# Kernel tuning notes

Measured on AMD Instinct MI355X. Metric: run time of the kernel, lower is better.

Reference implementation:

```python
import jax, jax.numpy as jnp
import numpy as np

EPS = 1e-12  # F.normalize eps

def _unfold3(x):
    # x: [B,C,H,W] -> [B, C*9, H*W], matching F.unfold(kernel=3, padding=1)
    B, C, H, W = x.shape
    xp = jnp.pad(x, ((0, 0), (0, 0), (1, 1), (1, 1)))
    pats = jnp.stack([xp[:, :, i:i + H, j:j + W]
                      for i in range(3) for j in range(3)], axis=2)  # [B,C,9,H,W]
    return pats.reshape(B, C * 9, H * W)

def _fold3(t, H, W):
    # inverse of _unfold3 with overlap-add, matching F.fold(kernel=3, padding=1)
    B, CK, L = t.shape
    C = CK // 9
    t = t.reshape(B, C, 3, 3, H, W)
    out = jnp.zeros((B, C, H + 2, W + 2), t.dtype)
    for i in range(3):
        for j in range(3):
            out = out.at[:, :, i:i + H, j:j + W].add(t[:, :, i, j])
    return out[:, :, 1:1 + H, 1:1 + W]

def setup_inputs() -> dict:
    key = jax.random.key(0)
    kV, kK, kQ = jax.random.split(key, 3)
    B, C, H, W = 4, 64, 64, 64
    return {
        'V': jax.random.normal(kV, (B, C, H, W), dtype=jnp.float32),
        'K': jax.random.normal(kK, (B, C, H, W), dtype=jnp.float32),
        'Q': jax.random.normal(kQ, (B, C, H, W), dtype=jnp.float32),
    }

def reference(V, K, Q):
    B, C, H, W = Q.shape
    Qu = _unfold3(Q)  # [B, C9, L]
    Ku = _unfold3(K)  # [B, C9, L]
    # F.normalize along the feature (C*9) axis for both K (after permute dim=2) and Q (dim=1)
    Kn = Ku / jnp.maximum(jnp.linalg.norm(Ku, axis=1, keepdims=True), EPS)
    Qn = Qu / jnp.maximum(jnp.linalg.norm(Qu, axis=1, keepdims=True), EPS)
    # R[b,k,q] = <Kn[b,:,k], Qn[b,:,q]>  -> [B, L, L]
    R = jnp.einsum('bfk,bfq->bkq', Kn, Qn)
    S = jnp.max(R, axis=1)        # [B, L]
    arg = jnp.argmax(R, axis=1)   # [B, L] best key patch per query position
    Vu = _unfold3(V)              # [B, C9, L]
    idx = jnp.broadcast_to(arg[:, None, :], Vu.shape)
    T_unfold = jnp.take_along_axis(Vu, idx, axis=2)  # gather along patch dim
    T = _fold3(T_unfold, H, W) / 9.0                 # [B, C, H, W]
    S = S.reshape(B, 1, H, W)
    return (S, T)
```

## Files before the change

### kernel.cpp

```cpp
#include <hip/hip_runtime.h>
#include <math.h>

#define HW 4096

typedef short bf16x8 __attribute__((ext_vector_type(8)));
typedef float floatx4 __attribute__((ext_vector_type(4)));
typedef unsigned short u16x8 __attribute__((ext_vector_type(8)));

__device__ __forceinline__ unsigned short f2bf_rne(float x) {
    unsigned int u = __float_as_uint(x);
    unsigned int r = (u + 0x7FFFu + ((u >> 16) & 1u)) >> 16;
    return (unsigned short)r;
}
__device__ __forceinline__ float bf2f(unsigned short h) {
    return __uint_as_float(((unsigned int)h) << 16);
}

__device__ __forceinline__ void gload_lds16(const void* gptr, void* lptr) {
    auto g = (const __attribute__((address_space(1))) unsigned int*)(unsigned long long)(gptr);
    auto l = (__attribute__((address_space(3))) unsigned int*)(unsigned int)(unsigned long long)(lptr);
    __builtin_amdgcn_global_load_lds(g, l, 16, 0, 0);
}

__global__ __launch_bounds__(256)
void prep_kernel(const float* __restrict__ Q, const float* __restrict__ K,
                 unsigned short* __restrict__ Aq, unsigned short* __restrict__ Bq,
                 float* __restrict__ pix2q, float* __restrict__ pix2k) {
    __shared__ float sT[64][65];
    const int tid = threadIdx.x;
    const int p0 = blockIdx.x * 64;
    const int b = blockIdx.y;
    const int isK = blockIdx.z;
    const float* __restrict__ src = isK ? K : Q;
    unsigned short* __restrict__ dst = isK ? Bq : Aq;
    float* __restrict__ pix2 = isK ? pix2k : pix2q;
    const int pp = tid >> 2, qt = tid & 3;
    const size_t base = ((size_t)b * 4096 + p0 + pp) * 192;

#pragma unroll
    for (int it = 0; it < 16; ++it) {
        int idx = it * 256 + tid;
        int c = idx >> 6, x = idx & 63;
        sT[c][x] = src[((size_t)b * 64 + c) * HW + p0 + x];
    }
    __syncthreads();
    {
        float sq = 0.f;
        u16x8 hv[2], lv[2];
#pragma unroll
        for (int g = 0; g < 2; ++g)
#pragma unroll
            for (int j = 0; j < 8; ++j) {
                int c = qt * 16 + g * 8 + j;
                float x = sT[c][pp];
                sq = fmaf(x, x, sq);
                unsigned short h = f2bf_rne(x);
                hv[g][j] = h;
                lv[g][j] = f2bf_rne(x - bf2f(h));
            }
        sq += __shfl_xor(sq, 1, 64);
        sq += __shfl_xor(sq, 2, 64);
        if (qt == 0) pix2[(b << 12) + p0 + pp] = sq;
#pragma unroll
        for (int g = 0; g < 2; ++g) {
            int co = qt * 16 + g * 8;
            *(u16x8*)(dst + base + co)       = hv[g];
            *(u16x8*)(dst + base + 64 + co)  = isK ? lv[g] : hv[g];
            *(u16x8*)(dst + base + 128 + co) = isK ? hv[g] : lv[g];
        }
    }
}

__global__ void patchnorm_kernel(const float* __restrict__ pix2q, const float* __restrict__ pix2k,
                                 float* __restrict__ rnq, float* __restrict__ rnk) {
    int idx = blockIdx.x * 256 + threadIdx.x;
    int b = idx >> 12, p = idx & 4095;
    int py = p >> 6, px = p & 63;
    float sq = 0.f, sk = 0.f;
    for (int dy = -1; dy <= 1; ++dy)
        for (int dx = -1; dx <= 1; ++dx) {
            int yy = py + dy, xx = px + dx;
            if ((unsigned)yy < 64u && (unsigned)xx < 64u) {
                int o = (b << 12) + (yy << 6) + xx;
                sq += pix2q[o];
                sk += pix2k[o];
            }
        }
    rnq[idx] = 1.f / fmaxf(sqrtf(sq), 1e-12f);
    rnk[idx] = 1.f / fmaxf(sqrtf(sk), 1e-12f);
}

#define WAITV(n_) asm volatile("s_waitcnt vmcnt(" #n_ ")" ::: "memory")
#define PBAR(n_) do { WAITV(n_); __builtin_amdgcn_s_barrier(); \
                      asm volatile("" ::: "memory"); } while (0)

#define ISSUE_A(c_, sg_, slot_) do { \
    const char* g_ = Aqb + (size_t)(q0 - 64 + (c_) * 64) * 384 + (sg_) * 128; \
    gload_lds16(g_ + g0off, smem + (slot_) * 8192 + l0off); \
    gload_lds16(g_ + g1off, smem + (slot_) * 8192 + l1off); \
} while (0)
#define ISSUE_B(c_, sg_, slot_) do { \
    const char* g_ = Bqb + (size_t)(k0 - 64 + (c_) * 64) * 384 + (sg_) * 128; \
    gload_lds16(g_ + g0off, smemB + (slot_) * 8192 + l0off); \
    gload_lds16(g_ + g1off, smemB + (slot_) * 8192 + l1off); \
} while (0)

#define MM16(af_, bfr_) do { \
    __builtin_amdgcn_s_setprio(1); \
    _Pragma("unroll") \
    for (int mt = 0; mt < 4; ++mt) \
        _Pragma("unroll") \
        for (int nt = 0; nt < 4; ++nt) \
            acc[mt][nt] = __builtin_amdgcn_mfma_f32_16x16x32_bf16( \
                (af_)[mt], (bfr_)[nt], acc[mt][nt], 0, 0, 0); \
    __builtin_amdgcn_s_setprio(0); \
} while (0)

#define STEP_S0(D_) do { \
    const char* As_ = smem + (wm + (D_)) * 8192; \
    const char* Bs_ = smemB + (wn + (D_)) * 8192; \
    _Pragma("unroll") \
    for (int kk = 0; kk < 2; ++kk) { \
        const int pk_ = kk ? posK1 : posK0; \
        _Pragma("unroll") \
        for (int mt = 0; mt < 4; ++mt) \
            afc[kk][mt] = *(const bf16x8*)(As_ + mt * 2048 + rowB + pk_); \
        _Pragma("unroll") \
        for (int nt = 0; nt < 4; ++nt) \
            bfc[kk][nt] = *(const bf16x8*)(Bs_ + nt * 2048 + rowB + pk_); \
        MM16(afc[kk], bfc[kk]); \
    } \
} while (0)

#define STEP_S1(D_) do { \
    const int xb_ = wn + (D_); \
    const char* Bs_ = smemB + (xb_ < 2 ? xb_ + 3 : xb_ - 2) * 8192; \
    _Pragma("unroll") \
    for (int kk = 0; kk < 2; ++kk) { \
        const int pk_ = kk ? posK1 : posK0; \
        bf16x8 bfr[4]; \
        _Pragma("unroll") \
        for (int nt = 0; nt < 4; ++nt) \
            bfr[nt] = *(const bf16x8*)(Bs_ + nt * 2048 + rowB + pk_); \
        MM16(afc[kk], bfr); \
    } \
} while (0)

#define STEP_S2(D_) do { \
    const int xa_ = wm + (D_); \
    const char* As_ = smem + ((xa_ & 1) ? (xa_ >> 1) : 4) * 8192; \
    _Pragma("unroll") \
    for (int kk = 0; kk < 2; ++kk) { \
        const int pk_ = kk ? posK1 : posK0; \
        bf16x8 af[4]; \
        _Pragma("unroll") \
        for (int mt = 0; mt < 4; ++mt) \
            af[mt] = *(const bf16x8*)(As_ + mt * 2048 + rowB + pk_); \
        MM16(af, bfc[kk]); \
    } \
} while (0)

__global__ __launch_bounds__(256, 2)
void gemm_fused_kernel(const unsigned short* __restrict__ Aq, const unsigned short* __restrict__ Bq,
                       const float* __restrict__ rnkA,
                       float* __restrict__ part_val, int* __restrict__ part_arg) {
    __shared__ __align__(16) char smem[81920];
    char* const smemB = smem + 40960;
    const int tid = threadIdx.x;
    const int lane = tid & 63, wid = tid >> 6;
    const int m15 = lane & 15, quad = lane >> 4;
    const int wm = wid & 1, wn = wid >> 1;
    const int f = blockIdx.x + (blockIdx.y << 5);
    const int o = ((f & 7) << 7) + (f >> 3);
    const int kt = o & 31, qt = o >> 5;
    const int k0 = kt << 7;
    const int q0 = qt << 7;
    const int b = blockIdx.z;
    const char* Aqb = (const char*)(Aq + (size_t)b * 4096 * 192);
    const char* Bqb = (const char*)(Bq + (size_t)b * 4096 * 192);
    const bool aInt = (q0 >= 64) && (q0 <= 4096 - 192);
    const bool bInt = (k0 >= 64) && (k0 <= 4096 - 192);

    const int rr0 = tid >> 3, ps = tid & 7;
    const int g0off = rr0 * 384 + (ps ^ (rr0 & 7)) * 16;
    const int l0off = tid * 16;
    const int rr1 = (256 + tid) >> 3;
    const int g1off = rr1 * 384 + (ps ^ (rr1 & 7)) * 16;
    const int l1off = (256 + tid) * 16;
    const int rowB = m15 * 128;
    const int posK0 = (quad ^ (m15 & 7)) * 16;
    const int posK1 = ((4 + quad) ^ (m15 & 7)) * 16;

    floatx4 acc[4][4];
#pragma unroll
    for (int i = 0; i < 4; ++i)
#pragma unroll
        for (int j = 0; j < 4; ++j) acc[i][j] = (floatx4)0.f;

    bf16x8 afc[2][4];
    bf16x8 bfc[2][4];

    if (aInt && bInt) {
        ISSUE_A(0, 0, 0); ISSUE_A(1, 0, 1); ISSUE_B(0, 0, 0); ISSUE_B(1, 0, 1);
        ISSUE_A(2, 0, 2); ISSUE_B(2, 0, 2); ISSUE_A(3, 0, 3); ISSUE_B(0, 1, 3);
        ISSUE_B(1, 1, 4); ISSUE_A(0, 2, 4);
        PBAR(12);                                      STEP_S0(0);
        PBAR(2);  ISSUE_A(1, 2, 0); ISSUE_B(2, 1, 0); STEP_S1(0);
        PBAR(2);  ISSUE_B(3, 0, 3);                   STEP_S2(0);
        PBAR(14); ISSUE_A(2, 2, 4);                   STEP_S0(1);
        PBAR(4);  ISSUE_B(3, 1, 1);                   STEP_S1(1);
        PBAR(2);  ISSUE_A(3, 2, 1);                   STEP_S2(1);
        PBAR(6);                                      STEP_S0(2);
        PBAR(2);                                      STEP_S1(2);
        PBAR(0);                                      STEP_S2(2);
        __syncthreads();
    } else {
        for (int seg = 0; seg < 3; ++seg) {
            const char* abL = Aqb + (size_t)(q0 - 64) * 384 + seg * 128;
            const char* bbL = Bqb + (size_t)(k0 - 64) * 384 + seg * 128;
            if (aInt) {
#pragma unroll
                for (int it = 0; it < 8; ++it) {
                    int slot = it * 256 + tid;
                    int row = slot >> 3, pos = slot & 7;
                    int G = pos ^ (row & 7);
                    gload_lds16(abL + (size_t)row * 384 + G * 16, smem + slot * 16);
                }
            } else {
#pragma unroll
                for (int it = 0; it < 8; ++it) {
                    int slot = it * 256 + tid;
                    int row = slot >> 3, pos = slot & 7;
                    int G = pos ^ (row & 7);
                    uint4 v = make_uint4(0u, 0u, 0u, 0u);
                    if ((unsigned)(q0 - 64 + row) < 4096u)
                        v = *(const uint4*)(abL + (size_t)row * 384 + G * 16);
                    *(uint4*)(smem + slot * 16) = v;
                }
            }
            if (bInt) {
#pragma unroll
                for (int it = 0; it < 8; ++it) {
                    int slot = it * 256 + tid;
                    int row = slot >> 3, pos = slot & 7;
                    int G = pos ^ (row & 7);
                    gload_lds16(bbL + (size_t)row * 384 + G * 16, smemB + slot * 16);
                }
            } else {
#pragma unroll
                for (int it = 0; it < 8; ++it) {
                    int slot = it * 256 + tid;
                    int row = slot >> 3, pos = slot & 7;
                    int G = pos ^ (row & 7);
                    uint4 v = make_uint4(0u, 0u, 0u, 0u);
                    if ((unsigned)(k0 - 64 + row) < 4096u)
                        v = *(const uint4*)(bbL + (size_t)row * 384 + G * 16);
                    *(uint4*)(smemB + slot * 16) = v;
                }
            }
            __syncthreads();
            STEP_S0(0); STEP_S0(1); STEP_S0(2);
            __syncthreads();
        }
    }

    float* Csh = (float*)smem;
    float* bvs = (float*)(smem + 34816);
    int*   bas = (int*)(smem + 35840);
    const int q_l = tid & 63;
    const int qr = tid >> 6;
    const int c0 = qr * 32;
    const float4 zero4 = make_float4(0.f, 0.f, 0.f, 0.f);

#pragma unroll
    for (int h = 0; h < 2; ++h) {
        if (h) __syncthreads();
        if (wm == h) {
#pragma unroll
            for (int mt = 0; mt < 4; ++mt)
#pragma unroll
                for (int nt = 0; nt < 4; ++nt)
#pragma unroll
                    for (int j = 0; j < 4; ++j)
                        Csh[(mt * 16 + quad * 4 + j) * 133 + wn * 64 + nt * 16 + m15] =
                            acc[mt][nt][j];
        }
        __syncthreads();

        const bool qm = q_l > 0;
        const bool qp = q_l < 63;
        const float* rC = Csh + q_l * 133;
        const float* rM = Csh + (q_l - 1) * 133;
        const float* rP = Csh + (q_l + 1) * 133;
        float4 prevm = (qm && c0 > 0) ? *(const float4*)&rM[c0 - 4] : zero4;
        float4 rpj   = qp ? *(const float4*)&rP[c0] : zero4;
        float bv = -INFINITY;
        int ba = 0;
#pragma unroll
        for (int j = 0; j < 8; ++j) {
            int c = c0 + 4 * j;
            float4 cen = *(const float4*)&rC[c];
            float4 rm4 = qm ? *(const float4*)&rM[c] : zero4;
            float4 rp1 = (qp && (c + 4) < 128) ? *(const float4*)&rP[c + 4] : zero4;
            float4 o4;
            o4.x = cen.x + (((c & 63) != 0) ? prevm.w : 0.f) + rpj.y;
            o4.y = cen.y + rm4.x + rpj.z;
            o4.z = cen.z + rm4.y + rpj.w;
            o4.w = cen.w + rm4.z + ((((c + 3) & 63) != 63) ? rp1.x : 0.f);
            float4 rk = *(const float4*)&rnkA[(b << 12) + k0 + c];
            float v0 = o4.x * rk.x; if (v0 > bv) { bv = v0; ba = k0 + c + 0; }
            float v1 = o4.y * rk.y; if (v1 > bv) { bv = v1; ba = k0 + c + 1; }
            float v2 = o4.z * rk.z; if (v2 > bv) { bv = v2; ba = k0 + c + 2; }
            float v3 = o4.w * rk.w; if (v3 > bv) { bv = v3; ba = k0 + c + 3; }
            prevm = rm4;
            rpj = rp1;
        }
        bvs[(qr << 6) + q_l] = bv;
        bas[(qr << 6) + q_l] = ba;
        __syncthreads();
        if (tid < 64) {
            float v = bvs[tid];
            int a = bas[tid];
#pragma unroll
            for (int s = 1; s < 4; ++s) {
                float v2 = bvs[(s << 6) + tid];
                if (v2 > v) { v = v2; a = bas[(s << 6) + tid]; }
            }
            int q = q0 + h * 64 + tid;
            part_val[(((b << 5) + kt) << 12) + q] = v;
            part_arg[(((b << 5) + kt) << 12) + q] = a;
        }
    }
}

__global__ __launch_bounds__(256)
void argcombine_kernel(const float* __restrict__ part_val, const int* __restrict__ part_arg,
                       const float* __restrict__ rnqA,
                       float* __restrict__ S_out, int* __restrict__ argF) {
    __shared__ float rv[4][64];
    __shared__ int ra[4][64];
    const int tid = threadIdx.x;
    const int qi = tid & 63, sg = tid >> 6;
    const int q = blockIdx.x * 64 + qi;
    const int b = blockIdx.y;
    const int base = (b << 17) + q;
    float bv = -INFINITY; int ba = 0;
#pragma unroll
    for (int s8 = 0; s8 < 8; ++s8) {
        int s = sg * 8 + s8;
        float v = part_val[base + (s << 12)];
        int aa = part_arg[base + (s << 12)];
        if (v > bv) { bv = v; ba = aa; }
    }
    rv[sg][qi] = bv; ra[sg][qi] = ba;
    __syncthreads();
    if (tid < 64) {
        float v = rv[0][tid]; int a = ra[0][tid];
#pragma unroll
        for (int s = 1; s < 4; ++s) {
            float v2 = rv[s][tid];
            if (v2 > v) { v = v2; a = ra[s][tid]; }
        }
        int idx = (b << 12) + blockIdx.x * 64 + tid;
        S_out[idx] = v * rnqA[idx];
        argF[idx] = a;
    }
}

__global__ __launch_bounds__(256)
void gatherT_kernel(const float* __restrict__ V, const int* __restrict__ argF,
                    float* __restrict__ T_out) {
    __shared__ int sArg[192];
    const int y = blockIdx.x, b = blockIdx.y, cg = blockIdx.z;
    const int tid = threadIdx.x;
    if (tid < 192) {
        int r = tid >> 6, x = tid & 63;
        int yy = y - 1 + r;
        sArg[tid] = ((unsigned)yy < 64u) ? argF[(b << 12) + (yy << 6) + x] : 0;
    }
    __syncthreads();

    const int x = tid & 63, cq = tid >> 6;
    int off[9];
#pragma unroll
    for (int t = 0; t < 9; ++t) {
        int dy = t / 3 - 1, dx = t % 3 - 1;
        int qy = y - dy, qx = x - dx;
        int o = -1;
        if ((unsigned)qy < 64u && (unsigned)qx < 64u) {
            int a = sArg[(1 - dy) * 64 + qx];
            int sy = (a >> 6) + dy, sx = (a & 63) + dx;
            if ((unsigned)sy < 64u && (unsigned)sx < 64u) o = (sy << 6) + sx;
        }
        off[t] = o;
    }
    const float* Vb = V + (size_t)b * 64 * HW;
    float* Tb = T_out + (size_t)b * 64 * HW + (y << 6) + x;
#pragma unroll
    for (int ci = 0; ci < 4; ++ci) {
        int c = cg * 16 + cq * 4 + ci;
        const float* Vc = Vb + (size_t)c * HW;
        float acc = 0.f;
#pragma unroll
        for (int t = 0; t < 9; ++t)
            acc += (off[t] >= 0) ? Vc[off[t]] : 0.f;
        Tb[(size_t)c * HW] = acc * (1.f / 9.f);
    }
}

extern "C" void kernel_launch(void* const* d_in, const int* in_sizes, int n_in,
                              void* d_out, int out_size, void* d_ws, size_t ws_size,
                              hipStream_t stream) {
    const float* V = (const float*)d_in[0];
    const float* K = (const float*)d_in[1];
    const float* Q = (const float*)d_in[2];
    float* S_out = (float*)d_out;
    float* T_out = S_out + 4 * HW;

    char* ws = (char*)d_ws;
    float* pix2q = (float*)(ws + 0);
    float* pix2k = (float*)(ws + 65536);
    float* rnq   = (float*)(ws + 131072);
    float* rnk   = (float*)(ws + 196608);
    float* part_val = (float*)(ws + 262144);
    int*   argF  = (int*)(ws + 4456448);
    int*   part_arg = (int*)(ws + 8650752);
    unsigned short* Aq = (unsigned short*)(ws + 17039360);
    unsigned short* Bq = (unsigned short*)(ws + 23330816);

    prep_kernel<<<dim3(64, 4, 2), 256, 0, stream>>>(Q, K, Aq, Bq, pix2q, pix2k);
    patchnorm_kernel<<<64, 256, 0, stream>>>(pix2q, pix2k, rnq, rnk);
    gemm_fused_kernel<<<dim3(32, 32, 4), 256, 0, stream>>>(Aq, Bq, rnk, part_val, part_arg);
    argcombine_kernel<<<dim3(64, 4), 256, 0, stream>>>(part_val, part_arg, rnq, S_out, argF);
    gatherT_kernel<<<dim3(64, 4, 4), 256, 0, stream>>>(V, argF, T_out);
}
```

Baseline: 201.9 us.

## Transpose V to pixel-major layout in prep and gather with float4 loads

After: 191.8 us. 5.0% less time.

```diff
diff --git a/kernel.cpp b/kernel.cpp
--- a/kernel.cpp
+++ b/kernel.cpp
@@ -24,18 +24,16 @@
 
 __global__ __launch_bounds__(256)
 void prep_kernel(const float* __restrict__ Q, const float* __restrict__ K,
+                 const float* __restrict__ V,
                  unsigned short* __restrict__ Aq, unsigned short* __restrict__ Bq,
+                 float* __restrict__ VT,
                  float* __restrict__ pix2q, float* __restrict__ pix2k) {
     __shared__ float sT[64][65];
     const int tid = threadIdx.x;
     const int p0 = blockIdx.x * 64;
     const int b = blockIdx.y;
-    const int isK = blockIdx.z;
-    const float* __restrict__ src = isK ? K : Q;
-    unsigned short* __restrict__ dst = isK ? Bq : Aq;
-    float* __restrict__ pix2 = isK ? pix2k : pix2q;
-    const int pp = tid >> 2, qt = tid & 3;
-    const size_t base = ((size_t)b * 4096 + p0 + pp) * 192;
+    const int which = blockIdx.z;
+    const float* __restrict__ src = (which == 0) ? Q : ((which == 1) ? K : V);
 
 #pragma unroll
     for (int it = 0; it < 16; ++it) {
@@ -44,6 +42,23 @@
         sT[c][x] = src[((size_t)b * 64 + c) * HW + p0 + x];
     }
     __syncthreads();
+    const int pp = tid >> 2, qt = tid & 3;
+
+    if (which == 2) {
+        float* dst = VT + ((size_t)b * 4096 + p0 + pp) * 64 + qt * 16;
+#pragma unroll
+        for (int j = 0; j < 4; ++j) {
+            float4 v = make_float4(sT[qt * 16 + 4 * j + 0][pp], sT[qt * 16 + 4 * j + 1][pp],
+                                   sT[qt * 16 + 4 * j + 2][pp], sT[qt * 16 + 4 * j + 3][pp]);
+            *(float4*)(dst + 4 * j) = v;
+        }
+        return;
+    }
+
+    const int isK = which;
+    unsigned short* __restrict__ dst = isK ? Bq : Aq;
+    float* __restrict__ pix2 = isK ? pix2k : pix2q;
+    const size_t base = ((size_t)b * 4096 + p0 + pp) * 192;
     {
         float sq = 0.f;
         u16x8 hv[2], lv[2];
@@ -368,7 +383,7 @@
 }
 
 __global__ __launch_bounds__(256)
-void gatherT_kernel(const float* __restrict__ V, const int* __restrict__ argF,
+void gatherT_kernel(const float* __restrict__ VT, const int* __restrict__ argF,
                     float* __restrict__ T_out) {
     __shared__ int sArg[192];
     const int y = blockIdx.x, b = blockIdx.y, cg = blockIdx.z;
@@ -380,32 +395,27 @@
     }
     __syncthreads();
 
-    const int x = tid & 63, cq = tid >> 6;
-    int off[9];
+    const int x = tid >> 2, cq = tid & 3;
+    const float* Vb = VT + (size_t)b * 4096 * 64 + cg * 16 + cq * 4;
+    float ax = 0.f, ay = 0.f, az = 0.f, aw = 0.f;
 #pragma unroll
     for (int t = 0; t < 9; ++t) {
         int dy = t / 3 - 1, dx = t % 3 - 1;
         int qy = y - dy, qx = x - dx;
-        int o = -1;
         if ((unsigned)qy < 64u && (unsigned)qx < 64u) {
             int a = sArg[(1 - dy) * 64 + qx];
             int sy = (a >> 6) + dy, sx = (a & 63) + dx;
-            if ((unsigned)sy < 64u && (unsigned)sx < 64u) o = (sy << 6) + sx;
-        }
-        off[t] = o;
-    }
-    const float* Vb = V + (size_t)b * 64 * HW;
-    float* Tb = T_out + (size_t)b * 64 * HW + (y << 6) + x;
-#pragma unroll
-    for (int ci = 0; ci < 4; ++ci) {
-        int c = cg * 16 + cq * 4 + ci;
-        const float* Vc = Vb + (size_t)c * HW;
-        float acc = 0.f;
-#pragma unroll
-        for (int t = 0; t < 9; ++t)
-            acc += (off[t] >= 0) ? Vc[off[t]] : 0.f;
-        Tb[(size_t)c * HW] = acc * (1.f / 9.f);
-    }
+            if ((unsigned)sy < 64u && (unsigned)sx < 64u) {
+                float4 v = *(const float4*)(Vb + (size_t)((sy << 6) + sx) * 64);
+                ax += v.x; ay += v.y; az += v.z; aw += v.w;
+            }
+        }
+    }
+    float* Tb = T_out + ((size_t)b * 64 + cg * 16 + cq * 4) * HW + (y << 6) + x;
+    Tb[0]          = ax * (1.f / 9.f);
+    Tb[HW]         = ay * (1.f / 9.f);
+    Tb[2 * HW]     = az * (1.f / 9.f);
+    Tb[3 * HW]     = aw * (1.f / 9.f);
 }
 
 extern "C" void kernel_launch(void* const* d_in, const int* in_sizes, int n_in,
@@ -425,12 +435,13 @@
     float* part_val = (float*)(ws + 262144);
     int*   argF  = (int*)(ws + 4456448);
     int*   part_arg = (int*)(ws + 8650752);
+    float* VT    = (float*)(ws + 10747904);
     unsigned short* Aq = (unsigned short*)(ws + 17039360);
     unsigned short* Bq = (unsigned short*)(ws + 23330816);
 
-    prep_kernel<<<dim3(64, 4, 2), 256, 0, stream>>>(Q, K, Aq, Bq, pix2q, pix2k);
+    prep_kernel<<<dim3(64, 4, 3), 256, 0, stream>>>(Q, K, V, Aq, Bq, VT, pix2q, pix2k);
     patchnorm_kernel<<<64, 256, 0, stream>>>(pix2q, pix2k, rnq, rnk);
     gemm_fused_kernel<<<dim3(32, 32, 4), 256, 0, stream>>>(Aq, Bq, rnk, part_val, part_arg);
     argcombine_kernel<<<dim3(64, 4), 256, 0, stream>>>(part_val, part_arg, rnq, S_out, argF);
-    gatherT_kernel<<<dim3(64, 4, 4), 256, 0, stream>>>(V, argF, T_out);
-}
+    gatherT_kernel<<<dim3(64, 4, 4), 256, 0, stream>>>(VT, argF, T_out);
+}
```
